# Performance work log

Measured on AMD Instinct MI355X. Metric: run time of the kernel, lower is better.

## Reference

```python
import jax, jax.numpy as jnp
import numpy as np

D_MODEL = 1024
NUM_HEADS = 16
D_K = D_MODEL // NUM_HEADS
B, L = 2, 4096


def setup_inputs() -> dict:
    key = jax.random.key(0)
    ks = jax.random.split(key, 12)
    s = 0.02
    return {
        "q": jax.random.normal(ks[0], (B, L, D_MODEL), dtype=jnp.float32),
        "k": jax.random.normal(ks[1], (B, L, D_MODEL), dtype=jnp.float32),
        "v": jax.random.normal(ks[2], (B, L, D_MODEL), dtype=jnp.float32),
        "Wq": jax.random.normal(ks[3], (D_MODEL, D_MODEL), dtype=jnp.float32) * s,
        "bq": jax.random.normal(ks[4], (D_MODEL,), dtype=jnp.float32) * s,
        "Wk": jax.random.normal(ks[5], (D_MODEL, D_MODEL), dtype=jnp.float32) * s,
        "bk": jax.random.normal(ks[6], (D_MODEL,), dtype=jnp.float32) * s,
        "Wv": jax.random.normal(ks[7], (D_MODEL, D_MODEL), dtype=jnp.float32) * s,
        "bv": jax.random.normal(ks[8], (D_MODEL,), dtype=jnp.float32) * s,
        "Wo": jax.random.normal(ks[9], (D_MODEL, D_MODEL), dtype=jnp.float32) * s,
        "bo": jax.random.normal(ks[10], (D_MODEL,), dtype=jnp.float32) * s,
    }


def reference(q, k, v, Wq, bq, Wk, bk, Wv, bv, Wo, bo):
    b, l, _ = q.shape
    # projections (torch Linear: x @ W.T + b), reshape to [b, l, h, d]
    qf = (q @ Wq.T + bq).reshape(b, l, NUM_HEADS, D_K)
    kf = (k @ Wk.T + bk).reshape(b, l, NUM_HEADS, D_K)
    vf = (v @ Wv.T + bv).reshape(b, l, NUM_HEADS, D_K)
    # elu+1 feature map (positive features)
    qf = jax.nn.elu(qf) + 1.0
    kf = jax.nn.elu(kf) + 1.0
    # normalizer uses full-sequence k sum (as in the original code)
    z = 1.0 / (jnp.einsum("blhd,bhd->blh", qf, kf.sum(axis=1)) + 1e-6)
    # cumulative sums over sequence (the linear-attention scan state)
    k_cum = jnp.cumsum(kf, axis=1)  # [b, l, h, d]
    v_cum = jnp.cumsum(vf, axis=1)  # [b, l, h, d]
    context = jnp.einsum("blhd,blhd->blh", qf, k_cum)  # [b, l, h]
    context = context[..., None] * v_cum * z[..., None]  # [b, l, h, d]
    context = context.reshape(b, l, NUM_HEADS * D_K)
    return context @ Wo.T + bo
```

## Files before the change

kernel.cpp:

```cpp
#include <hip/hip_runtime.h>
#include <hip/hip_bf16.h>
#include <cstdint>
#include <cstddef>

#define D_MODEL 1024
#define NUM_HEADS 16
#define DK_DIM 64
#define BATCH 2
#define SEQ 4096
#define MROWS (BATCH*SEQ)
#define NCHUNK 128
#define CHUNK 32

#define BM 256
#define BN 128
#define BK 64
#define NSLOT 3
#define SLOT_SH (BM*BK + BN*BK)
#define KTILES (D_MODEL/BK)

typedef __attribute__((ext_vector_type(4))) float f32x4;
typedef __attribute__((ext_vector_type(2))) float f32x2;
typedef __attribute__((ext_vector_type(8))) short bf16x8;
typedef __attribute__((ext_vector_type(4))) short s16x4;
typedef __attribute__((ext_vector_type(2))) uint32_t u32x2;
typedef __attribute__((ext_vector_type(4))) uint32_t u32x4;

__device__ __forceinline__ float b2f(short s) {
  union { uint32_t u; float f; } c; c.u = ((uint32_t)(uint16_t)s) << 16; return c.f;
}
__device__ __forceinline__ short f2b(float f) {
  union { float f; uint32_t u; } c; c.f = f;
  uint32_t u = c.u;
  u += 0x7FFFu + ((u >> 16) & 1u);
  return (short)(u >> 16);
}
__device__ __forceinline__ f32x4 b4_to_f4(s16x4 s) {
  f32x4 r;
  r.x = b2f(s.x); r.y = b2f(s.y); r.z = b2f(s.z); r.w = b2f(s.w);
  return r;
}
__device__ __forceinline__ uint32_t cvtpk(float lo, float hi) {
  uint32_t r;
  asm("v_cvt_pk_bf16_f32 %0, %1, %2" : "=v"(r) : "v"(lo), "v"(hi));
  return r;
}

__global__ __launch_bounds__(256) void cvt_w4(
    const float* __restrict__ s0, const float* __restrict__ s1,
    const float* __restrict__ s2, const float* __restrict__ s3,
    short* __restrict__ dst) {
  const int y = blockIdx.y;
  const float* s = (y == 0) ? s0 : (y == 1) ? s1 : (y == 2) ? s2 : s3;
  s16x4* d = reinterpret_cast<s16x4*>(dst) + (size_t)y * (D_MODEL * D_MODEL / 4);
  const int n4 = D_MODEL * D_MODEL / 4;
  for (int i = blockIdx.x * 256 + threadIdx.x; i < n4; i += 128 * 256) {
    float4 v = reinterpret_cast<const float4*>(s)[i];
    s16x4 o;
    o.x = f2b(v.x); o.y = f2b(v.y); o.z = f2b(v.z); o.w = f2b(v.w);
    d[i] = o;
  }
}

__global__ __launch_bounds__(256) void cvt_in3(
    const float* __restrict__ s0, const float* __restrict__ s1,
    const float* __restrict__ s2, short* __restrict__ dst) {
  const int y = blockIdx.y;
  const float* s = (y == 0) ? s0 : (y == 1) ? s1 : s2;
  s16x4* d = reinterpret_cast<s16x4*>(dst) + (size_t)y * (MROWS * D_MODEL / 4);
  const int n4 = MROWS * D_MODEL / 4;
  for (int i = blockIdx.x * 256 + threadIdx.x; i < n4; i += 512 * 256) {
    float4 v = reinterpret_cast<const float4*>(s)[i];
    s16x4 o;
    o.x = f2b(v.x); o.y = f2b(v.y); o.z = f2b(v.z); o.w = f2b(v.w);
    d[i] = o;
  }
}

template<int OUTBF16, int CSUM>
__global__ __launch_bounds__(512, 2) void gemm8(
    const void* __restrict__ A0, const void* __restrict__ A1,
    const void* __restrict__ A2, const short* __restrict__ Wbase,
    const float* __restrict__ b0, const float* __restrict__ b1,
    const float* __restrict__ b2, void* __restrict__ Cbase, int actmask,
    float* __restrict__ ckp, float* __restrict__ cvp)
{
  extern __shared__ __align__(16) short lds[];
  const int tid = threadIdx.x;
  const int wid = tid >> 6;
  const int lane = tid & 63;
  const int brow = blockIdx.x * BM;
  const int bcol = blockIdx.y * BN;
  const int z = blockIdx.z;
  const int wr = wid >> 1, wc = wid & 1;

  const void* Ap = (z == 0) ? A0 : (z == 1) ? A1 : A2;
  const float* bias = (z == 0) ? b0 : (z == 1) ? b1 : b2;
  const short* Bw = Wbase + (size_t)z * D_MODEL * D_MODEL;
  const int act = (actmask >> z) & 1;
  const short* __restrict__ A16 = (const short*)Ap;

  f32x4 acc[4][4];
#pragma unroll
  for (int i = 0; i < 4; ++i)
#pragma unroll
    for (int j = 0; j < 4; ++j)
#pragma unroll
      for (int t = 0; t < 4; ++t) acc[i][j][t] = 0.f;

  const int srow = lane >> 3;
  const int gql  = lane & 7;
  const int sgel = (gql ^ srow) * 8;

  auto stageB = [&](int t) {
    short* sB = lds + (t % NSLOT) * SLOT_SH + BM * BK;
    const int k0 = t * BK;
#pragma unroll
    for (int i = 0; i < 2; ++i) {
      const int r = i * 64 + wid * 8;
      const short* g = Bw + (size_t)(bcol + r + srow) * D_MODEL + k0 + sgel;
      __builtin_amdgcn_global_load_lds((const __attribute__((address_space(1))) void*)g,
          (__attribute__((address_space(3))) void*)(sB + r * BK), 16, 0, 0);
    }
  };
  auto stageA16 = [&](int t) {
    short* sA = lds + (t % NSLOT) * SLOT_SH;
    const int k0 = t * BK;
#pragma unroll
    for (int i = 0; i < 4; ++i) {
      const int r = i * 64 + wid * 8;
      const short* g = A16 + (size_t)(brow + r + srow) * D_MODEL + k0 + sgel;
      __builtin_amdgcn_global_load_lds((const __attribute__((address_space(1))) void*)g,
          (__attribute__((address_space(3))) void*)(sA + r * BK), 16, 0, 0);
    }
  };

  const int lane15 = lane & 15;
  const int swz = (lane & 7) << 4;
  const int kq = (lane >> 4) * 16;

  auto compute = [&](int t) {
    const char* sAb = (const char*)(lds + (t % NSLOT) * SLOT_SH);
    const char* sBb = sAb + BM * BK * 2;
    auto rdA = [&](int mi, int ks) -> bf16x8 {
      const int row = wr * 64 + mi * 16 + lane15;
      const int off = row * 128 + ((ks * 64 + kq) ^ swz);
      return *reinterpret_cast<const bf16x8*>(sAb + off);
    };
    auto rdB = [&](int nj, int ks) -> bf16x8 {
      const int row = wc * 64 + nj * 16 + lane15;
      const int off = row * 128 + ((ks * 64 + kq) ^ swz);
      return *reinterpret_cast<const bf16x8*>(sBb + off);
    };
    bf16x8 Af[2][2], Bf[2][2][2];
#pragma unroll
    for (int m2 = 0; m2 < 2; ++m2)
#pragma unroll
      for (int ks = 0; ks < 2; ++ks) Af[m2][ks] = rdA(m2, ks);
#pragma unroll
    for (int j2 = 0; j2 < 2; ++j2)
#pragma unroll
      for (int ks = 0; ks < 2; ++ks) Bf[0][j2][ks] = rdB(j2, ks);
#pragma unroll
    for (int m2 = 0; m2 < 2; ++m2)
#pragma unroll
      for (int j2 = 0; j2 < 2; ++j2)
#pragma unroll
        for (int ks = 0; ks < 2; ++ks)
          acc[m2][j2] = __builtin_amdgcn_mfma_f32_16x16x32_bf16(Bf[0][j2][ks], Af[m2][ks], acc[m2][j2], 0, 0, 0);
#pragma unroll
    for (int j2 = 0; j2 < 2; ++j2)
#pragma unroll
      for (int ks = 0; ks < 2; ++ks) Bf[1][j2][ks] = rdB(2 + j2, ks);
#pragma unroll
    for (int m2 = 0; m2 < 2; ++m2)
#pragma unroll
      for (int j2 = 0; j2 < 2; ++j2)
#pragma unroll
        for (int ks = 0; ks < 2; ++ks)
          acc[m2][2 + j2] = __builtin_amdgcn_mfma_f32_16x16x32_bf16(Bf[1][j2][ks], Af[m2][ks], acc[m2][2 + j2], 0, 0, 0);
#pragma unroll
    for (int m2 = 0; m2 < 2; ++m2)
#pragma unroll
      for (int ks = 0; ks < 2; ++ks) Af[m2][ks] = rdA(2 + m2, ks);
#pragma unroll
    for (int m2 = 0; m2 < 2; ++m2)
#pragma unroll
      for (int j2 = 0; j2 < 2; ++j2)
#pragma unroll
        for (int ks = 0; ks < 2; ++ks)
          acc[2 + m2][2 + j2] = __builtin_amdgcn_mfma_f32_16x16x32_bf16(Bf[1][j2][ks], Af[m2][ks], acc[2 + m2][2 + j2], 0, 0, 0);
#pragma unroll
    for (int m2 = 0; m2 < 2; ++m2)
#pragma unroll
      for (int j2 = 0; j2 < 2; ++j2)
#pragma unroll
        for (int ks = 0; ks < 2; ++ks)
          acc[2 + m2][j2] = __builtin_amdgcn_mfma_f32_16x16x32_bf16(Bf[0][j2][ks], Af[m2][ks], acc[2 + m2][j2], 0, 0, 0);
  };

  stageA16(0); stageB(0);
  stageA16(1); stageB(1);
#pragma unroll 1
  for (int t = 0; t < KTILES; ++t) {
    if (t == KTILES - 1) { asm volatile("s_waitcnt vmcnt(0)" ::: "memory"); }
    else                 { asm volatile("s_waitcnt vmcnt(6)" ::: "memory"); }
    __builtin_amdgcn_s_barrier();
    __builtin_amdgcn_sched_barrier(0);
    if (t + 2 < KTILES) { stageA16(t + 2); stageB(t + 2); }
    compute(t);
  }

  const int csub4 = (lane >> 4) * 4;
  f32x4 csum[2][4];
  if constexpr (CSUM) {
#pragma unroll
    for (int cp = 0; cp < 2; ++cp)
#pragma unroll
      for (int nj = 0; nj < 4; ++nj)
#pragma unroll
        for (int t = 0; t < 4; ++t) csum[cp][nj][t] = 0.f;
  }
#pragma unroll
  for (int mi = 0; mi < 4; ++mi) {
    const int row = brow + wr * 64 + mi * 16 + lane15;
    const size_t rowbase = (size_t)z * MROWS * D_MODEL + (size_t)row * D_MODEL;
#pragma unroll
    for (int nj = 0; nj < 4; ++nj) {
      const int col0 = bcol + wc * 64 + nj * 16 + csub4;
      const float4 bv = *reinterpret_cast<const float4*>(&bias[col0]);
      float v0 = acc[mi][nj][0] + bv.x;
      float v1 = acc[mi][nj][1] + bv.y;
      float v2 = acc[mi][nj][2] + bv.z;
      float v3 = acc[mi][nj][3] + bv.w;
      if (act) {
        v0 = (v0 > 0.f) ? (v0 + 1.f) : __expf(v0);
        v1 = (v1 > 0.f) ? (v1 + 1.f) : __expf(v1);
        v2 = (v2 > 0.f) ? (v2 + 1.f) : __expf(v2);
        v3 = (v3 > 0.f) ? (v3 + 1.f) : __expf(v3);
      }
      if constexpr (CSUM) {
        csum[mi >> 1][nj][0] += v0;
        csum[mi >> 1][nj][1] += v1;
        csum[mi >> 1][nj][2] += v2;
        csum[mi >> 1][nj][3] += v3;
      }
      if (OUTBF16) {
        u32x2 w;
        w.x = cvtpk(v0, v1);
        w.y = cvtpk(v2, v3);
        *reinterpret_cast<u32x2*>(&((short*)Cbase)[rowbase + col0]) = w;
      } else {
        float4 w; w.x = v0; w.y = v1; w.z = v2; w.w = v3;
        *reinterpret_cast<float4*>(&((float*)Cbase)[rowbase + col0]) = w;
      }
    }
  }
  if constexpr (CSUM) {
    if (z >= 1) {
      float* dst = (z == 1) ? ckp : cvp;
      const int b  = brow >> 12;
      const int l0 = brow & (SEQ - 1);
      const int h  = (bcol >> 6) + wc;
      const int bh = b * NUM_HEADS + h;
#pragma unroll
      for (int cp = 0; cp < 2; ++cp) {
#pragma unroll
        for (int nj = 0; nj < 4; ++nj) {
          f32x4 s = csum[cp][nj];
#pragma unroll
          for (int m = 1; m < 16; m <<= 1) {
            s[0] += __shfl_xor(s[0], m, 64);
            s[1] += __shfl_xor(s[1], m, 64);
            s[2] += __shfl_xor(s[2], m, 64);
            s[3] += __shfl_xor(s[3], m, 64);
          }
          if (lane15 == 0) {
            const int cg = (l0 >> 5) + wr * 2 + cp;
            const int d0 = nj * 16 + csub4;
            *reinterpret_cast<f32x4*>(
                &dst[((size_t)(bh * NCHUNK + cg)) * DK_DIM + d0]) = s;
          }
        }
      }
    }
  }
}

__global__ __launch_bounds__(64) void chunk_scan(
    float* __restrict__ ck, float* __restrict__ cv, float* __restrict__ ksum)
{
  const int bh = blockIdx.x;
  const int d = threadIdx.x;
  float rk = 0.f, rv = 0.f;
#pragma unroll 8
  for (int c = 0; c < NCHUNK; ++c) {
    const size_t o = ((size_t)(bh * NCHUNK + c)) * DK_DIM + d;
    const float tk = ck[o], tv = cv[o];
    ck[o] = rk; cv[o] = rv;
    rk += tk; rv += tv;
  }
  ksum[bh * DK_DIM + d] = rk;
}

__global__ __launch_bounds__(256) void scan_ctx(
    const short* __restrict__ qf, const short* __restrict__ kf,
    const short* __restrict__ vf,
    const float* __restrict__ ck, const float* __restrict__ cv,
    const float* __restrict__ ksum, short* __restrict__ ctx)
{
  const int gw = blockIdx.x * 4 + (threadIdx.x >> 6);
  const int lane = threadIdx.x & 63;
  const int pg = lane >> 4;
  const int dg = lane & 15;
  const int c = gw & (NCHUNK - 1);
  const int h = (gw >> 7) & (NUM_HEADS - 1);
  const int b = gw >> 11;
  const int bh = b * NUM_HEADS + h;
  const int d4 = dg * 4;

  f32x4 krun = *reinterpret_cast<const f32x4*>(
      &ck[((size_t)(bh * NCHUNK + c)) * DK_DIM + d4]);
  f32x4 vrun = *reinterpret_cast<const f32x4*>(
      &cv[((size_t)(bh * NCHUNK + c)) * DK_DIM + d4]);
  const f32x4 kst = *reinterpret_cast<const f32x4*>(&ksum[bh * DK_DIM + d4]);

  const size_t base = ((size_t)(b * SEQ + c * CHUNK) * NUM_HEADS + h) * DK_DIM + d4;

  for (int p0 = 0; p0 < CHUNK; p0 += 4) {
    const size_t qoff = base + (size_t)(p0 + pg) * D_MODEL;
    const f32x4 q4 = b4_to_f4(*reinterpret_cast<const s16x4*>(&qf[qoff]));
    f32x4 sk, sv;
#pragma unroll
    for (int i = 0; i < 4; ++i) {
      const size_t off = base + (size_t)(p0 + i) * D_MODEL;
      krun += b4_to_f4(*reinterpret_cast<const s16x4*>(&kf[off]));
      vrun += b4_to_f4(*reinterpret_cast<const s16x4*>(&vf[off]));
      if (i == pg) { sk = krun; sv = vrun; }
    }
    float s1 = q4.x * sk.x + q4.y * sk.y + q4.z * sk.z + q4.w * sk.w;
    float s2 = q4.x * kst.x + q4.y * kst.y + q4.z * kst.z + q4.w * kst.w;
#pragma unroll
    for (int m = 1; m < 16; m <<= 1) {
      s1 += __shfl_xor(s1, m, 64);
      s2 += __shfl_xor(s2, m, 64);
    }
    const float g = s1 / (s2 + 1e-6f);
    s16x4 o;
    o.x = f2b(g * sv.x); o.y = f2b(g * sv.y);
    o.z = f2b(g * sv.z); o.w = f2b(g * sv.w);
    *reinterpret_cast<s16x4*>(&ctx[qoff]) = o;
  }
}

extern "C" void kernel_launch(void* const* d_in, const int* in_sizes, int n_in,
                              void* d_out, int out_size, void* d_ws, size_t ws_size,
                              hipStream_t stream) {
  const float* q  = (const float*)d_in[0];
  const float* k  = (const float*)d_in[1];
  const float* v  = (const float*)d_in[2];
  const float* Wq = (const float*)d_in[3];
  const float* bq = (const float*)d_in[4];
  const float* Wk = (const float*)d_in[5];
  const float* bk = (const float*)d_in[6];
  const float* Wv = (const float*)d_in[7];
  const float* bv = (const float*)d_in[8];
  const float* Wo = (const float*)d_in[9];
  const float* bo = (const float*)d_in[10];
  float* out = (float*)d_out;

  uint8_t* p = (uint8_t*)d_ws;
  auto alloc = [&](size_t bytes) { uint8_t* r = p; p += bytes; return r; };
  short* qf  = (short*)alloc((size_t)MROWS * D_MODEL * 2);
  short* kf  = (short*)alloc((size_t)MROWS * D_MODEL * 2);
  short* vf  = (short*)alloc((size_t)MROWS * D_MODEL * 2);
  short* ctx = (short*)alloc((size_t)MROWS * D_MODEL * 2);
  short* qb  = (short*)alloc((size_t)MROWS * D_MODEL * 2);
  short* kb  = (short*)alloc((size_t)MROWS * D_MODEL * 2);
  short* vb  = (short*)alloc((size_t)MROWS * D_MODEL * 2);
  short* Wqb = (short*)alloc((size_t)D_MODEL * D_MODEL * 2);
  short* Wkb = (short*)alloc((size_t)D_MODEL * D_MODEL * 2);
  short* Wvb = (short*)alloc((size_t)D_MODEL * D_MODEL * 2);
  short* Wob = (short*)alloc((size_t)D_MODEL * D_MODEL * 2);
  float* ck   = (float*)alloc((size_t)BATCH * NUM_HEADS * NCHUNK * DK_DIM * 4);
  float* cv   = (float*)alloc((size_t)BATCH * NUM_HEADS * NCHUNK * DK_DIM * 4);
  float* ksum = (float*)alloc((size_t)BATCH * NUM_HEADS * DK_DIM * 4);
  (void)Wkb; (void)Wvb; (void)kb; (void)vb;

  const dim3 gproj(MROWS / BM, D_MODEL / BN, 3);
  const dim3 gout (MROWS / BM, D_MODEL / BN, 1);
  const int shbytes = NSLOT * SLOT_SH * (int)sizeof(short);

  (void)hipFuncSetAttribute((const void*)gemm8<1, 1>,
      hipFuncAttributeMaxDynamicSharedMemorySize, shbytes);
  (void)hipFuncSetAttribute((const void*)gemm8<0, 0>,
      hipFuncAttributeMaxDynamicSharedMemorySize, shbytes);

  cvt_w4<<<dim3(128, 4), 256, 0, stream>>>(Wq, Wk, Wv, Wo, Wqb);
  cvt_in3<<<dim3(512, 3), 256, 0, stream>>>(q, k, v, qb);

  gemm8<1, 1><<<gproj, 512, shbytes, stream>>>(qb, kb, vb, Wqb, bq, bk, bv, qf, 0x3, ck, cv);

  chunk_scan<<<BATCH * NUM_HEADS, 64, 0, stream>>>(ck, cv, ksum);
  scan_ctx<<<BATCH * NUM_HEADS * NCHUNK / 4, 256, 0, stream>>>(qf, kf, vf, ck, cv, ksum, ctx);

  gemm8<0, 0><<<gout, 512, shbytes, stream>>>(ctx, ctx, ctx, Wob, bo, bo, bo, out, 0, nullptr, nullptr);
}
```

Baseline: 152.9 us.

## Shrink GEMM tile to 128x128 with 4 waves, double buffering, merged convert kernel

```diff
diff --git a/kernel.cpp b/kernel.cpp
--- a/kernel.cpp
+++ b/kernel.cpp
@@ -12,19 +12,16 @@
 #define NCHUNK 128
 #define CHUNK 32
 
-#define BM 256
+#define BM 128
 #define BN 128
 #define BK 64
-#define NSLOT 3
-#define SLOT_SH (BM*BK + BN*BK)
+#define SLOT_SH ((BM+BN)*BK)
 #define KTILES (D_MODEL/BK)
 
 typedef __attribute__((ext_vector_type(4))) float f32x4;
-typedef __attribute__((ext_vector_type(2))) float f32x2;
 typedef __attribute__((ext_vector_type(8))) short bf16x8;
 typedef __attribute__((ext_vector_type(4))) short s16x4;
 typedef __attribute__((ext_vector_type(2))) uint32_t u32x2;
-typedef __attribute__((ext_vector_type(4))) uint32_t u32x4;
 
 __device__ __forceinline__ float b2f(short s) {
   union { uint32_t u; float f; } c; c.u = ((uint32_t)(uint16_t)s) << 16; return c.f;
@@ -46,39 +43,35 @@
   return r;
 }
 
-__global__ __launch_bounds__(256) void cvt_w4(
-    const float* __restrict__ s0, const float* __restrict__ s1,
-    const float* __restrict__ s2, const float* __restrict__ s3,
-    short* __restrict__ dst) {
+__global__ __launch_bounds__(256) void cvt7(
+    const float* __restrict__ Wq, const float* __restrict__ Wk,
+    const float* __restrict__ Wv, const float* __restrict__ Wo,
+    const float* __restrict__ q, const float* __restrict__ k,
+    const float* __restrict__ v,
+    short* __restrict__ wdst, short* __restrict__ idst) {
   const int y = blockIdx.y;
-  const float* s = (y == 0) ? s0 : (y == 1) ? s1 : (y == 2) ? s2 : s3;
-  s16x4* d = reinterpret_cast<s16x4*>(dst) + (size_t)y * (D_MODEL * D_MODEL / 4);
-  const int n4 = D_MODEL * D_MODEL / 4;
-  for (int i = blockIdx.x * 256 + threadIdx.x; i < n4; i += 128 * 256) {
-    float4 v = reinterpret_cast<const float4*>(s)[i];
+  const float* s;
+  s16x4* d;
+  int n4;
+  if (y < 4) {
+    s = (y == 0) ? Wq : (y == 1) ? Wk : (y == 2) ? Wv : Wo;
+    d = reinterpret_cast<s16x4*>(wdst) + (size_t)y * (D_MODEL * D_MODEL / 4);
+    n4 = D_MODEL * D_MODEL / 4;
+  } else {
+    s = (y == 4) ? q : (y == 5) ? k : v;
+    d = reinterpret_cast<s16x4*>(idst) + (size_t)(y - 4) * (MROWS * D_MODEL / 4);
+    n4 = MROWS * D_MODEL / 4;
+  }
+  for (int i = blockIdx.x * 256 + threadIdx.x; i < n4; i += 256 * 256) {
+    float4 vv = reinterpret_cast<const float4*>(s)[i];
     s16x4 o;
-    o.x = f2b(v.x); o.y = f2b(v.y); o.z = f2b(v.z); o.w = f2b(v.w);
+    o.x = f2b(vv.x); o.y = f2b(vv.y); o.z = f2b(vv.z); o.w = f2b(vv.w);
     d[i] = o;
   }
 }
 
-__global__ __launch_bounds__(256) void cvt_in3(
-    const float* __restrict__ s0, const float* __restrict__ s1,
-    const float* __restrict__ s2, short* __restrict__ dst) {
-  const int y = blockIdx.y;
-  const float* s = (y == 0) ? s0 : (y == 1) ? s1 : s2;
-  s16x4* d = reinterpret_cast<s16x4*>(dst) + (size_t)y * (MROWS * D_MODEL / 4);
-  const int n4 = MROWS * D_MODEL / 4;
-  for (int i = blockIdx.x * 256 + threadIdx.x; i < n4; i += 512 * 256) {
-    float4 v = reinterpret_cast<const float4*>(s)[i];
-    s16x4 o;
-    o.x = f2b(v.x); o.y = f2b(v.y); o.z = f2b(v.z); o.w = f2b(v.w);
-    d[i] = o;
-  }
-}
-
 template<int OUTBF16, int CSUM>
-__global__ __launch_bounds__(512, 2) void gemm8(
+__global__ __launch_bounds__(256, 2) void gemm4d(
     const void* __restrict__ A0, const void* __restrict__ A1,
     const void* __restrict__ A2, const short* __restrict__ Wbase,
     const float* __restrict__ b0, const float* __restrict__ b1,
@@ -94,11 +87,10 @@
   const int z = blockIdx.z;
   const int wr = wid >> 1, wc = wid & 1;
 
-  const void* Ap = (z == 0) ? A0 : (z == 1) ? A1 : A2;
+  const short* A16 = (const short*)((z == 0) ? A0 : (z == 1) ? A1 : A2);
   const float* bias = (z == 0) ? b0 : (z == 1) ? b1 : b2;
   const short* Bw = Wbase + (size_t)z * D_MODEL * D_MODEL;
   const int act = (actmask >> z) & 1;
-  const short* __restrict__ A16 = (const short*)Ap;
 
   f32x4 acc[4][4];
 #pragma unroll
@@ -112,103 +104,61 @@
   const int gql  = lane & 7;
   const int sgel = (gql ^ srow) * 8;
 
-  auto stageB = [&](int t) {
-    short* sB = lds + (t % NSLOT) * SLOT_SH + BM * BK;
+  auto stage = [&](int t, int slot) {
+    short* sA = lds + slot * SLOT_SH;
+    short* sB = sA + BM * BK;
     const int k0 = t * BK;
 #pragma unroll
-    for (int i = 0; i < 2; ++i) {
-      const int r = i * 64 + wid * 8;
+    for (int i = 0; i < 4; ++i) {
+      const int r = i * 32 + wid * 8;
+      const short* g = A16 + (size_t)(brow + r + srow) * D_MODEL + k0 + sgel;
+      __builtin_amdgcn_global_load_lds((const __attribute__((address_space(1))) void*)g,
+          (__attribute__((address_space(3))) void*)(sA + r * BK), 16, 0, 0);
+    }
+#pragma unroll
+    for (int i = 0; i < 4; ++i) {
+      const int r = i * 32 + wid * 8;
       const short* g = Bw + (size_t)(bcol + r + srow) * D_MODEL + k0 + sgel;
       __builtin_amdgcn_global_load_lds((const __attribute__((address_space(1))) void*)g,
           (__attribute__((address_space(3))) void*)(sB + r * BK), 16, 0, 0);
     }
   };
-  auto stageA16 = [&](int t) {
-    short* sA = lds + (t % NSLOT) * SLOT_SH;
-    const int k0 = t * BK;
-#pragma unroll
-    for (int i = 0; i < 4; ++i) {
-      const int r = i * 64 + wid * 8;
-      const short* g = A16 + (size_t)(brow + r + srow) * D_MODEL + k0 + sgel;
-      __builtin_amdgcn_global_load_lds((const __attribute__((address_space(1))) void*)g,
-          (__attribute__((address_space(3))) void*)(sA + r * BK), 16, 0, 0);
-    }
-  };
 
   const int lane15 = lane & 15;
   const int swz = (lane & 7) << 4;
   const int kq = (lane >> 4) * 16;
 
-  auto compute = [&](int t) {
-    const char* sAb = (const char*)(lds + (t % NSLOT) * SLOT_SH);
+  auto compute = [&](int slot) {
+    const char* sAb = (const char*)(lds + slot * SLOT_SH);
     const char* sBb = sAb + BM * BK * 2;
-    auto rdA = [&](int mi, int ks) -> bf16x8 {
-      const int row = wr * 64 + mi * 16 + lane15;
-      const int off = row * 128 + ((ks * 64 + kq) ^ swz);
-      return *reinterpret_cast<const bf16x8*>(sAb + off);
-    };
-    auto rdB = [&](int nj, int ks) -> bf16x8 {
-      const int row = wc * 64 + nj * 16 + lane15;
-      const int off = row * 128 + ((ks * 64 + kq) ^ swz);
-      return *reinterpret_cast<const bf16x8*>(sBb + off);
-    };
-    bf16x8 Af[2][2], Bf[2][2][2];
-#pragma unroll
-    for (int m2 = 0; m2 < 2; ++m2)
-#pragma unroll
-      for (int ks = 0; ks < 2; ++ks) Af[m2][ks] = rdA(m2, ks);
-#pragma unroll
-    for (int j2 = 0; j2 < 2; ++j2)
-#pragma unroll
-      for (int ks = 0; ks < 2; ++ks) Bf[0][j2][ks] = rdB(j2, ks);
-#pragma unroll
-    for (int m2 = 0; m2 < 2; ++m2)
-#pragma unroll
-      for (int j2 = 0; j2 < 2; ++j2)
-#pragma unroll
-        for (int ks = 0; ks < 2; ++ks)
-          acc[m2][j2] = __builtin_amdgcn_mfma_f32_16x16x32_bf16(Bf[0][j2][ks], Af[m2][ks], acc[m2][j2], 0, 0, 0);
-#pragma unroll
-    for (int j2 = 0; j2 < 2; ++j2)
-#pragma unroll
-      for (int ks = 0; ks < 2; ++ks) Bf[1][j2][ks] = rdB(2 + j2, ks);
-#pragma unroll
-    for (int m2 = 0; m2 < 2; ++m2)
-#pragma unroll
-      for (int j2 = 0; j2 < 2; ++j2)
-#pragma unroll
-        for (int ks = 0; ks < 2; ++ks)
-          acc[m2][2 + j2] = __builtin_amdgcn_mfma_f32_16x16x32_bf16(Bf[1][j2][ks], Af[m2][ks], acc[m2][2 + j2], 0, 0, 0);
-#pragma unroll
-    for (int m2 = 0; m2 < 2; ++m2)
-#pragma unroll
-      for (int ks = 0; ks < 2; ++ks) Af[m2][ks] = rdA(2 + m2, ks);
-#pragma unroll
-    for (int m2 = 0; m2 < 2; ++m2)
-#pragma unroll
-      for (int j2 = 0; j2 < 2; ++j2)
-#pragma unroll
-        for (int ks = 0; ks < 2; ++ks)
-          acc[2 + m2][2 + j2] = __builtin_amdgcn_mfma_f32_16x16x32_bf16(Bf[1][j2][ks], Af[m2][ks], acc[2 + m2][2 + j2], 0, 0, 0);
-#pragma unroll
-    for (int m2 = 0; m2 < 2; ++m2)
-#pragma unroll
-      for (int j2 = 0; j2 < 2; ++j2)
-#pragma unroll
-        for (int ks = 0; ks < 2; ++ks)
-          acc[2 + m2][j2] = __builtin_amdgcn_mfma_f32_16x16x32_bf16(Bf[0][j2][ks], Af[m2][ks], acc[2 + m2][j2], 0, 0, 0);
+#pragma unroll
+    for (int ks = 0; ks < 2; ++ks) {
+      bf16x8 Af[4], Bf[4];
+#pragma unroll
+      for (int mi = 0; mi < 4; ++mi)
+        Af[mi] = *reinterpret_cast<const bf16x8*>(
+            sAb + (wr * 64 + mi * 16 + lane15) * 128 + ((ks * 64 + kq) ^ swz));
+#pragma unroll
+      for (int nj = 0; nj < 4; ++nj)
+        Bf[nj] = *reinterpret_cast<const bf16x8*>(
+            sBb + (wc * 64 + nj * 16 + lane15) * 128 + ((ks * 64 + kq) ^ swz));
+#pragma unroll
+      for (int mi = 0; mi < 4; ++mi)
+#pragma unroll
+        for (int nj = 0; nj < 4; ++nj)
+          acc[mi][nj] = __builtin_amdgcn_mfma_f32_16x16x32_bf16(Bf[nj], Af[mi], acc[mi][nj], 0, 0, 0);
+    }
   };
 
-  stageA16(0); stageB(0);
-  stageA16(1); stageB(1);
+  stage(0, 0);
 #pragma unroll 1
   for (int t = 0; t < KTILES; ++t) {
-    if (t == KTILES - 1) { asm volatile("s_waitcnt vmcnt(0)" ::: "memory"); }
-    else                 { asm volatile("s_waitcnt vmcnt(6)" ::: "memory"); }
+    const int cur = t & 1;
+    asm volatile("s_waitcnt vmcnt(0)" ::: "memory");
     __builtin_amdgcn_s_barrier();
     __builtin_amdgcn_sched_barrier(0);
-    if (t + 2 < KTILES) { stageA16(t + 2); stageB(t + 2); }
-    compute(t);
+    if (t + 1 < KTILES) stage(t + 1, cur ^ 1);
+    compute(cur);
   }
 
   const int csub4 = (lane >> 4) * 4;
@@ -389,20 +339,19 @@
 
   const dim3 gproj(MROWS / BM, D_MODEL / BN, 3);
   const dim3 gout (MROWS / BM, D_MODEL / BN, 1);
-  const int shbytes = NSLOT * SLOT_SH * (int)sizeof(short);
-
-  (void)hipFuncSetAttribute((const void*)gemm8<1, 1>,
+  const int shbytes = 2 * SLOT_SH * (int)sizeof(short);
+
+  (void)hipFuncSetAttribute((const void*)gemm4d<1, 1>,
       hipFuncAttributeMaxDynamicSharedMemorySize, shbytes);
-  (void)hipFuncSetAttribute((const void*)gemm8<0, 0>,
+  (void)hipFuncSetAttribute((const void*)gemm4d<0, 0>,
       hipFuncAttributeMaxDynamicSharedMemorySize, shbytes);
 
-  cvt_w4<<<dim3(128, 4), 256, 0, stream>>>(Wq, Wk, Wv, Wo, Wqb);
-  cvt_in3<<<dim3(512, 3), 256, 0, stream>>>(q, k, v, qb);
-
-  gemm8<1, 1><<<gproj, 512, shbytes, stream>>>(qb, kb, vb, Wqb, bq, bk, bv, qf, 0x3, ck, cv);
+  cvt7<<<dim3(256, 7), 256, 0, stream>>>(Wq, Wk, Wv, Wo, q, k, v, Wqb, qb);
+
+  gemm4d<1, 1><<<gproj, 256, shbytes, stream>>>(qb, kb, vb, Wqb, bq, bk, bv, qf, 0x3, ck, cv);
 
   chunk_scan<<<BATCH * NUM_HEADS, 64, 0, stream>>>(ck, cv, ksum);
   scan_ctx<<<BATCH * NUM_HEADS * NCHUNK / 4, 256, 0, stream>>>(qf, kf, vf, ck, cv, ksum, ctx);
 
-  gemm8<0, 0><<<gout, 512, shbytes, stream>>>(ctx, ctx, ctx, Wob, bo, bo, bo, out, 0, nullptr, nullptr);
-}
+  gemm4d<0, 0><<<gout, 256, shbytes, stream>>>(ctx, ctx, ctx, Wob, bo, bo, bo, out, 0, nullptr, nullptr);
+}
```

Measured after the change: 151.9 us. Within noise of the previous version (-0.6%).
